# Kernel tuning notes

Hardware: AMD Instinct MI355X
Metric: run time of the kernel (lower is better)

The kernel has to match this reference:

```python
import jax, jax.numpy as jnp
import numpy as np

T, IN_DIM, HID, OUT = 4096, 768, 768, 4

def setup_inputs() -> dict:
    key = jax.random.key(0)
    ks = jax.random.split(key, 5)
    s_i = 1.0 / np.sqrt(IN_DIM)
    s_h = 1.0 / np.sqrt(HID)
    return {
        "inputs": jax.random.normal(ks[0], (T, IN_DIM), jnp.float32),
        "h0": jnp.zeros((HID,), jnp.float32),
        "Wi": jax.random.normal(ks[1], (IN_DIM, 3 * HID), jnp.float32) * s_i,
        "bi": jnp.zeros((3 * HID,), jnp.float32),
        "Wh": jax.random.normal(ks[2], (HID, 3 * HID), jnp.float32) * s_h,
        "bhn": jnp.zeros((HID,), jnp.float32),
        "Wd": jax.random.normal(ks[3], (HID, OUT), jnp.float32) * s_h,
        "bd": jnp.zeros((OUT,), jnp.float32),
    }

def reference(inputs, h0, Wi, bi, Wh, bhn, Wd, bd):
    H = h0.shape[-1]
    # Precompute all input projections in one big GEMM: [T, 3H]
    xi_all = inputs @ Wi + bi

    def step(h, xi):
        hh = h @ Wh  # [3H]
        xr, xz, xn = xi[:H], xi[H:2 * H], xi[2 * H:]
        hr, hz, hn = hh[:H], hh[H:2 * H], hh[2 * H:]
        r = jax.nn.sigmoid(xr + hr)
        z = jax.nn.sigmoid(xz + hz)
        n = jnp.tanh(xn + r * (hn + bhn))
        h_new = (1.0 - z) * n + z * h  # flax GRUCell update
        return h_new, h_new

    final_h, y = jax.lax.scan(step, h0, xi_all)  # y: [T, H]
    output = y @ Wd + bd  # [T, OUT]
    rng = jax.random.key(42)
    rng, act_rng = jax.random.split(rng)
    action = jax.random.categorical(act_rng, output[:, :2])  # [T]
    return output, action, final_h
```

## Files before the change

### kernel.cpp

```cpp
#include <hip/hip_runtime.h>
#include <stdint.h>

#define T_STEPS 4096
#define HID     768
#define G3      2304
#define NBLK    192
#define NTHR    192
#define UPB     4

__device__ __forceinline__ void threefry2x32(uint32_t k0, uint32_t k1,
                                             uint32_t x0, uint32_t x1,
                                             uint32_t* o0, uint32_t* o1) {
  uint32_t ks0 = k0, ks1 = k1, ks2 = k0 ^ k1 ^ 0x1BD11BDAu;
  uint32_t ks[3] = {ks0, ks1, ks2};
  x0 += ks[0]; x1 += ks[1];
  const int r0[4] = {13, 15, 26, 6};
  const int r1[4] = {17, 29, 16, 24};
#pragma unroll
  for (int i = 0; i < 5; ++i) {
    const int* rr = (i & 1) ? r1 : r0;
#pragma unroll
    for (int j = 0; j < 4; ++j) {
      x0 += x1;
      x1 = (x1 << rr[j]) | (x1 >> (32 - rr[j]));
      x1 ^= x0;
    }
    x0 += ks[(i + 1) % 3];
    x1 += ks[(i + 2) % 3] + (uint32_t)(i + 1);
  }
  *o0 = x0; *o1 = x1;
}

__device__ __forceinline__ float gumbel_from_bits(uint32_t bits) {
  float f = __uint_as_float((bits >> 9) | 0x3f800000u) - 1.0f;
  float u = fmaxf(f, 1.17549435e-38f);
  return -logf(-logf(u));
}

__global__ void init_pairs(const float* __restrict__ h0,
                           unsigned long long* __restrict__ pairs) {
  int j = threadIdx.x;
  if (j < HID) {
    pairs[j]        = (unsigned long long)__float_as_uint(h0[j]);
    pairs[HID + j]  = 0xFFFFFFFF00000000ull;
  }
}

__launch_bounds__(256)
__global__ void gemm_xi(const float* __restrict__ A, const float* __restrict__ B,
                        const float* __restrict__ bias, float* __restrict__ C) {
  const int M = T_STEPS, N = G3, K = HID;
  (void)M;
  __shared__ __align__(16) float As[8][128];
  __shared__ __align__(16) float Bs[8][128];
  int tid = threadIdx.x;
  int bn = blockIdx.x * 128;
  int bm = blockIdx.y * 128;
  int tx = tid & 15, ty = tid >> 4;

  float acc[8][8];
#pragma unroll
  for (int i = 0; i < 8; ++i)
#pragma unroll
    for (int j = 0; j < 8; ++j) acc[i][j] = 0.f;

  const int ar = tid >> 1;
  const int ac = (tid & 1) * 4;
  const int br = tid >> 5;
  const int bc = (tid & 31) * 4;
  const float* Aptr = A + (size_t)(bm + ar) * K + ac;
  const float* Bptr = B + (size_t)br * N + bn + bc;

  for (int k0 = 0; k0 < K; k0 += 8) {
    float4 av = *(const float4*)(Aptr + k0);
    float4 bv = *(const float4*)(Bptr + (size_t)k0 * N);
    As[ac + 0][ar] = av.x; As[ac + 1][ar] = av.y;
    As[ac + 2][ar] = av.z; As[ac + 3][ar] = av.w;
    *(float4*)&Bs[br][bc] = bv;
    __syncthreads();
#pragma unroll
    for (int kk = 0; kk < 8; ++kk) {
      float a[8], b[8];
      *(float4*)&a[0] = *(const float4*)&As[kk][ty * 8];
      *(float4*)&a[4] = *(const float4*)&As[kk][ty * 8 + 4];
      *(float4*)&b[0] = *(const float4*)&Bs[kk][tx * 8];
      *(float4*)&b[4] = *(const float4*)&Bs[kk][tx * 8 + 4];
#pragma unroll
      for (int i = 0; i < 8; ++i)
#pragma unroll
        for (int j = 0; j < 8; ++j) acc[i][j] = fmaf(a[i], b[j], acc[i][j]);
    }
    __syncthreads();
  }
#pragma unroll
  for (int i = 0; i < 8; ++i) {
    float* crow = C + (size_t)(bm + ty * 8 + i) * N + bn + tx * 8;
    const float* brow = bias + bn + tx * 8;
#pragma unroll
    for (int j = 0; j < 8; ++j) crow[j] = acc[i][j] + brow[j];
  }
}

__launch_bounds__(NTHR)
__global__ void gru_scan(const float* __restrict__ xi, const float* __restrict__ Wh,
                         const float* __restrict__ bhn,
                         unsigned long long* __restrict__ pairs,
                         float* __restrict__ y) {
  __shared__ __align__(16) float h_lds[16 * 52];
  __shared__ float dots[12];

  const int tid = threadIdx.x;
  const int b = blockIdx.x;
  const int g = tid >> 4;
  const int l = tid & 15;
  const int u0 = b * UPB;

  const int C = (g < 4) ? (u0 + g)
              : (g < 8) ? (HID + u0 + (g - 4))
                        : (2 * HID + u0 + (g - 8));

  float w[48];
#pragma unroll
  for (int i = 0; i < 48; ++i) w[i] = Wh[(size_t)(l * 48 + i) * G3 + C];

  float bhn_u = 0.f;
  if (tid < UPB) bhn_u = bhn[u0 + tid];

  const int base_k = tid * 4;

  for (int t = 0; t < T_STEPS; ++t) {
    unsigned long long* buf = pairs + (size_t)(t & 1) * HID;

    float xr = 0.f, xz = 0.f, xn = 0.f;
    if (tid < UPB) {
      const float* xrow = xi + (size_t)t * G3;
      xr = xrow[u0 + tid];
      xz = xrow[HID + u0 + tid];
      xn = xrow[2 * HID + u0 + tid];
    }

    unsigned int got = 0;
    while (got != 0xFu) {
#pragma unroll
      for (int c = 0; c < 4; ++c) {
        if (!(got & (1u << c))) {
          unsigned long long v = __hip_atomic_load(&buf[base_k + c], __ATOMIC_RELAXED,
                                                   __HIP_MEMORY_SCOPE_AGENT);
          if ((int)(v >> 32) == t) {
            int k = base_k + c;
            h_lds[k + 4 * (k / 48)] = __uint_as_float((unsigned int)v);
            got |= (1u << c);
          }
        }
      }
    }
    __syncthreads();

    float a0 = 0.f, a1 = 0.f, a2 = 0.f, a3 = 0.f;
    const float4* hp = (const float4*)&h_lds[52 * l];
#pragma unroll
    for (int i = 0; i < 12; ++i) {
      float4 h4 = hp[i];
      a0 = fmaf(w[4 * i + 0], h4.x, a0);
      a1 = fmaf(w[4 * i + 1], h4.y, a1);
      a2 = fmaf(w[4 * i + 2], h4.z, a2);
      a3 = fmaf(w[4 * i + 3], h4.w, a3);
    }
    float acc = (a0 + a1) + (a2 + a3);
    acc += __shfl_xor(acc, 8, 16);
    acc += __shfl_xor(acc, 4, 16);
    acc += __shfl_xor(acc, 2, 16);
    acc += __shfl_xor(acc, 1, 16);
    if (l == 0) dots[g] = acc;

    float hprev = 0.f;
    if (tid < UPB) {
      int j = u0 + tid;
      hprev = h_lds[j + 4 * (j / 48)];
    }
    __syncthreads();

    if (tid < UPB) {
      float hr = dots[tid], hz = dots[4 + tid], hn = dots[8 + tid];
      float r = 1.f / (1.f + expf(-(xr + hr)));
      float z = 1.f / (1.f + expf(-(xz + hz)));
      float n = tanhf(xn + r * (hn + bhn_u));
      float hnew = (1.f - z) * n + z * hprev;
      int j = u0 + tid;
      y[(size_t)t * HID + j] = hnew;
      unsigned long long pv =
          (((unsigned long long)(unsigned int)(t + 1)) << 32) | __float_as_uint(hnew);
      __hip_atomic_store(&pairs[(size_t)((t + 1) & 1) * HID + j], pv, __ATOMIC_RELAXED,
                         __HIP_MEMORY_SCOPE_AGENT);
    }
    __syncthreads();
  }
}

__launch_bounds__(256)
__global__ void decode_out(const float* __restrict__ y, const float* __restrict__ Wd,
                           const float* __restrict__ bd, float* __restrict__ out) {
  int tid = threadIdx.x;
  int lane = tid & 63;
  int wid = tid >> 6;
  int r = blockIdx.x * 4 + wid;
  const float* yr = y + (size_t)r * HID;

  float acc0 = 0.f, acc1 = 0.f, acc2 = 0.f, acc3 = 0.f;
#pragma unroll
  for (int i = 0; i < 12; ++i) {
    int k = lane + 64 * i;
    float yv = yr[k];
    float4 wd = *(const float4*)&Wd[(size_t)k * 4];
    acc0 = fmaf(yv, wd.x, acc0);
    acc1 = fmaf(yv, wd.y, acc1);
    acc2 = fmaf(yv, wd.z, acc2);
    acc3 = fmaf(yv, wd.w, acc3);
    if (r == T_STEPS - 1) out[20480 + k] = yv;
  }
#pragma unroll
  for (int m = 32; m >= 1; m >>= 1) {
    acc0 += __shfl_xor(acc0, m, 64);
    acc1 += __shfl_xor(acc1, m, 64);
    acc2 += __shfl_xor(acc2, m, 64);
    acc3 += __shfl_xor(acc3, m, 64);
  }
  if (lane == 0) {
    float o0 = acc0 + bd[0], o1 = acc1 + bd[1], o2 = acc2 + bd[2], o3 = acc3 + bd[3];
    out[(size_t)r * 4 + 0] = o0;
    out[(size_t)r * 4 + 1] = o1;
    out[(size_t)r * 4 + 2] = o2;
    out[(size_t)r * 4 + 3] = o3;

    uint32_t ak0, ak1;
    threefry2x32(0u, 42u, 0u, 1u, &ak0, &ak1);

    uint32_t s0, s1;
    threefry2x32(ak0, ak1, 0u, (uint32_t)(2 * r), &s0, &s1);
    uint32_t g0bits = s0 ^ s1;
    threefry2x32(ak0, ak1, 0u, (uint32_t)(2 * r + 1), &s0, &s1);
    uint32_t g1bits = s0 ^ s1;

    float gg0 = gumbel_from_bits(g0bits);
    float gg1 = gumbel_from_bits(g1bits);
    int action = (o1 + gg1 > o0 + gg0) ? 1 : 0;
    out[16384 + r] = (float)action;
  }
}

extern "C" void kernel_launch(void* const* d_in, const int* in_sizes, int n_in,
                              void* d_out, int out_size, void* d_ws, size_t ws_size,
                              hipStream_t stream) {
  const float* inputs = (const float*)d_in[0];
  const float* h0     = (const float*)d_in[1];
  const float* Wi     = (const float*)d_in[2];
  const float* bi     = (const float*)d_in[3];
  const float* Wh     = (const float*)d_in[4];
  const float* bhn    = (const float*)d_in[5];
  const float* Wd     = (const float*)d_in[6];
  const float* bd     = (const float*)d_in[7];
  float* out = (float*)d_out;

  char* ws = (char*)d_ws;
  unsigned long long* pairs = (unsigned long long*)ws;
  float* xi = (float*)(ws + 16384);
  float* y  = (float*)(ws + 16384 + (size_t)T_STEPS * G3 * 4);

  hipLaunchKernelGGL(init_pairs, dim3(1), dim3(HID), 0, stream, h0, pairs);
  hipLaunchKernelGGL(gemm_xi, dim3(G3 / 128, T_STEPS / 128), dim3(256), 0, stream,
                     inputs, Wi, bi, xi);

  {
    const float* xi_c = xi;
    const float* wh_c = Wh;
    const float* bhn_c = bhn;
    unsigned long long* pr = pairs;
    float* y_p = y;
    void* args[] = { (void*)&xi_c, (void*)&wh_c, (void*)&bhn_c, (void*)&pr, (void*)&y_p };
    hipError_t e = hipLaunchCooperativeKernel((const void*)gru_scan, dim3(NBLK),
                                              dim3(NTHR), args, 0, stream);
    if (e != hipSuccess) {
      hipLaunchKernelGGL(gru_scan, dim3(NBLK), dim3(NTHR), 0, stream,
                         xi_c, wh_c, bhn_c, pr, y_p);
    }
  }

  hipLaunchKernelGGL(decode_out, dim3(T_STEPS / 4), dim3(256), 0, stream, y, Wd, bd, out);
}
```

Measured before the change: 10.67 ms.

## Restructure GRU scan to one wavefront per unit without LDS or block barriers

The recurrent scan kernel now gives each hidden unit its own 64-lane wavefront. Every lane polls 12 elements of the shared h buffer directly from global memory, keeps h in registers, and does all three gate dot-products with a full-wave shuffle reduction. This removes the LDS staging and the three __syncthreads per timestep, so each wavefront proceeds independently. In exchange, every wavefront polls the whole 768-entry h vector each step, which multiplies global atomic-load traffic by four, and the block grows to 256 threads.

Result: slower. 20.24 ms (+89.7%).

```diff
diff --git a/kernel.cpp b/kernel.cpp
--- a/kernel.cpp
+++ b/kernel.cpp
@@ -5,7 +5,7 @@
 #define HID     768
 #define G3      2304
 #define NBLK    192
-#define NTHR    192
+#define NTHR    256
 #define UPB     4
 
 __device__ __forceinline__ void threefry2x32(uint32_t k0, uint32_t k1,
@@ -49,8 +49,7 @@
 __launch_bounds__(256)
 __global__ void gemm_xi(const float* __restrict__ A, const float* __restrict__ B,
                         const float* __restrict__ bias, float* __restrict__ C) {
-  const int M = T_STEPS, N = G3, K = HID;
-  (void)M;
+  const int N = G3, K = HID;
   __shared__ __align__(16) float As[8][128];
   __shared__ __align__(16) float Bs[8][128];
   int tid = threadIdx.x;
@@ -103,97 +102,78 @@
 
 __launch_bounds__(NTHR)
 __global__ void gru_scan(const float* __restrict__ xi, const float* __restrict__ Wh,
-                         const float* __restrict__ bhn,
+                         const float* __restrict__ bhn, const float* __restrict__ h0,
                          unsigned long long* __restrict__ pairs,
                          float* __restrict__ y) {
-  __shared__ __align__(16) float h_lds[16 * 52];
-  __shared__ float dots[12];
-
-  const int tid = threadIdx.x;
-  const int b = blockIdx.x;
-  const int g = tid >> 4;
-  const int l = tid & 15;
-  const int u0 = b * UPB;
-
-  const int C = (g < 4) ? (u0 + g)
-              : (g < 8) ? (HID + u0 + (g - 4))
-                        : (2 * HID + u0 + (g - 8));
-
-  float w[48];
-#pragma unroll
-  for (int i = 0; i < 48; ++i) w[i] = Wh[(size_t)(l * 48 + i) * G3 + C];
-
-  float bhn_u = 0.f;
-  if (tid < UPB) bhn_u = bhn[u0 + tid];
-
-  const int base_k = tid * 4;
+  const int tid  = threadIdx.x;
+  const int lane = tid & 63;
+  const int u    = tid >> 6;
+  const int unit = blockIdx.x * UPB + u;
+
+  const int c_r = unit;
+  const int c_z = HID + unit;
+  const int c_n = 2 * HID + unit;
+
+  float wr[12], wz[12], wn[12];
+#pragma unroll
+  for (int i = 0; i < 12; ++i) {
+    int row = 64 * i + lane;
+    wr[i] = Wh[(size_t)row * G3 + c_r];
+    wz[i] = Wh[(size_t)row * G3 + c_z];
+    wn[i] = Wh[(size_t)row * G3 + c_n];
+  }
+  const float bhn_u = bhn[unit];
+  float h_cur = h0[unit];
 
   for (int t = 0; t < T_STEPS; ++t) {
-    unsigned long long* buf = pairs + (size_t)(t & 1) * HID;
-
-    float xr = 0.f, xz = 0.f, xn = 0.f;
-    if (tid < UPB) {
-      const float* xrow = xi + (size_t)t * G3;
-      xr = xrow[u0 + tid];
-      xz = xrow[HID + u0 + tid];
-      xn = xrow[2 * HID + u0 + tid];
-    }
-
-    unsigned int got = 0;
-    while (got != 0xFu) {
-#pragma unroll
-      for (int c = 0; c < 4; ++c) {
-        if (!(got & (1u << c))) {
-          unsigned long long v = __hip_atomic_load(&buf[base_k + c], __ATOMIC_RELAXED,
-                                                   __HIP_MEMORY_SCOPE_AGENT);
-          if ((int)(v >> 32) == t) {
-            int k = base_k + c;
-            h_lds[k + 4 * (k / 48)] = __uint_as_float((unsigned int)v);
-            got |= (1u << c);
-          }
-        }
-      }
-    }
-    __syncthreads();
-
-    float a0 = 0.f, a1 = 0.f, a2 = 0.f, a3 = 0.f;
-    const float4* hp = (const float4*)&h_lds[52 * l];
+    const unsigned long long* buf = pairs + (size_t)(t & 1) * HID;
+
+    const float* xrow = xi + (size_t)t * G3;
+    float xr_v = xrow[c_r];
+    float xz_v = xrow[c_z];
+    float xn_v = xrow[c_n];
+
+    unsigned long long v[12];
+    bool need = true;
+    while (need) {
+#pragma unroll
+      for (int i = 0; i < 12; ++i)
+        v[i] = __hip_atomic_load(&buf[64 * i + lane], __ATOMIC_RELAXED,
+                                 __HIP_MEMORY_SCOPE_AGENT);
+      bool ok = true;
+#pragma unroll
+      for (int i = 0; i < 12; ++i)
+        ok &= ((unsigned int)(v[i] >> 32) == (unsigned int)t);
+      need = !ok;
+    }
+
+    float ar = 0.f, az = 0.f, an = 0.f;
 #pragma unroll
     for (int i = 0; i < 12; ++i) {
-      float4 h4 = hp[i];
-      a0 = fmaf(w[4 * i + 0], h4.x, a0);
-      a1 = fmaf(w[4 * i + 1], h4.y, a1);
-      a2 = fmaf(w[4 * i + 2], h4.z, a2);
-      a3 = fmaf(w[4 * i + 3], h4.w, a3);
-    }
-    float acc = (a0 + a1) + (a2 + a3);
-    acc += __shfl_xor(acc, 8, 16);
-    acc += __shfl_xor(acc, 4, 16);
-    acc += __shfl_xor(acc, 2, 16);
-    acc += __shfl_xor(acc, 1, 16);
-    if (l == 0) dots[g] = acc;
-
-    float hprev = 0.f;
-    if (tid < UPB) {
-      int j = u0 + tid;
-      hprev = h_lds[j + 4 * (j / 48)];
-    }
-    __syncthreads();
-
-    if (tid < UPB) {
-      float hr = dots[tid], hz = dots[4 + tid], hn = dots[8 + tid];
-      float r = 1.f / (1.f + expf(-(xr + hr)));
-      float z = 1.f / (1.f + expf(-(xz + hz)));
-      float n = tanhf(xn + r * (hn + bhn_u));
-      float hnew = (1.f - z) * n + z * hprev;
-      int j = u0 + tid;
-      y[(size_t)t * HID + j] = hnew;
+      float hv = __uint_as_float((unsigned int)v[i]);
+      ar = fmaf(hv, wr[i], ar);
+      az = fmaf(hv, wz[i], az);
+      an = fmaf(hv, wn[i], an);
+    }
+#pragma unroll
+    for (int m = 1; m < 64; m <<= 1) {
+      ar += __shfl_xor(ar, m, 64);
+      az += __shfl_xor(az, m, 64);
+      an += __shfl_xor(an, m, 64);
+    }
+
+    if (lane == 0) {
+      float r = 1.f / (1.f + expf(-(xr_v + ar)));
+      float z = 1.f / (1.f + expf(-(xz_v + az)));
+      float n = tanhf(xn_v + r * (an + bhn_u));
+      float hnew = (1.f - z) * n + z * h_cur;
+      h_cur = hnew;
+      y[(size_t)t * HID + unit] = hnew;
       unsigned long long pv =
           (((unsigned long long)(unsigned int)(t + 1)) << 32) | __float_as_uint(hnew);
-      __hip_atomic_store(&pairs[(size_t)((t + 1) & 1) * HID + j], pv, __ATOMIC_RELAXED,
-                         __HIP_MEMORY_SCOPE_AGENT);
-    }
-    __syncthreads();
+      __hip_atomic_store(&pairs[(size_t)((t + 1) & 1) * HID + unit], pv,
+                         __ATOMIC_RELAXED, __HIP_MEMORY_SCOPE_AGENT);
+    }
   }
 }
 
@@ -234,7 +214,6 @@
 
     uint32_t ak0, ak1;
     threefry2x32(0u, 42u, 0u, 1u, &ak0, &ak1);
-
     uint32_t s0, s1;
     threefry2x32(ak0, ak1, 0u, (uint32_t)(2 * r), &s0, &s1);
     uint32_t g0bits = s0 ^ s1;
@@ -274,14 +253,16 @@
     const float* xi_c = xi;
     const float* wh_c = Wh;
     const float* bhn_c = bhn;
+    const float* h0_c = h0;
     unsigned long long* pr = pairs;
     float* y_p = y;
-    void* args[] = { (void*)&xi_c, (void*)&wh_c, (void*)&bhn_c, (void*)&pr, (void*)&y_p };
+    void* args[] = { (void*)&xi_c, (void*)&wh_c, (void*)&bhn_c, (void*)&h0_c,
+                     (void*)&pr, (void*)&y_p };
     hipError_t e = hipLaunchCooperativeKernel((const void*)gru_scan, dim3(NBLK),
                                               dim3(NTHR), args, 0, stream);
     if (e != hipSuccess) {
       hipLaunchKernelGGL(gru_scan, dim3(NBLK), dim3(NTHR), 0, stream,
-                         xi_c, wh_c, bhn_c, pr, y_p);
+                         xi_c, wh_c, bhn_c, h0_c, pr, y_p);
     }
   }
 
```
